# Kernel tuning notes

Hardware: AMD Instinct MI355X
Metric: run time of the kernel (lower is better)

## Reference

```python
import jax, jax.numpy as jnp
import numpy as np

N_HEAD = 8

def setup_inputs() -> dict:
    key = jax.random.key(0)
    ks = jax.random.split(key, 5)
    B, T, C = 2, 4096, 512
    x = jax.random.normal(ks[0], (B, T, C), dtype=jnp.float32)
    w_attn = jax.random.normal(ks[1], (3 * C, C), dtype=jnp.float32) * (1.0 / np.sqrt(C))
    b_attn = jax.random.normal(ks[2], (3 * C,), dtype=jnp.float32) * 0.02
    w_proj = jax.random.normal(ks[3], (C, C), dtype=jnp.float32) * (1.0 / np.sqrt(C))
    b_proj = jax.random.normal(ks[4], (C,), dtype=jnp.float32) * 0.02
    return {"x": x, "w_attn": w_attn, "b_attn": b_attn, "w_proj": w_proj, "b_proj": b_proj}

def reference(x, w_attn, b_attn, w_proj, b_proj):
    B, T, C = x.shape
    H = N_HEAD
    D = C // H  # head dim
    qkv = x @ w_attn.T + b_attn  # [B,T,3C]
    q, k, v = jnp.split(qkv, 3, axis=-1)
    # b t (h d) -> b h t d
    def to_heads(t):
        return t.reshape(B, T, H, D).transpose(0, 2, 1, 3)
    q, k, v = to_heads(q), to_heads(k), to_heads(v)
    scale = 1.0 / np.sqrt(D).astype(np.float32)
    att = jnp.einsum('bhqd,bhkd->bhqk', q, k) * scale  # [B,H,T,T]
    causal = jnp.tril(jnp.ones((T, T), dtype=bool))
    att = jnp.where(causal[None, None], att, jnp.float32(-jnp.inf))
    att = jax.nn.softmax(att, axis=-1)
    y = jnp.einsum('bhqk,bhkd->bhqd', att, v)  # [B,H,T,D]
    y = y.transpose(0, 2, 1, 3).reshape(B, T, C)
    return y @ w_proj.T + b_proj
```

## Files before the change

kernel.cpp:

```cpp
#include <hip/hip_runtime.h>

typedef __attribute__((ext_vector_type(8))) __bf16 bf16x8;
typedef __attribute__((ext_vector_type(4))) __bf16 bf16x4;
typedef __attribute__((ext_vector_type(4))) float f32x4;
typedef __attribute__((ext_vector_type(16))) float f32x16;
typedef __attribute__((ext_vector_type(4))) unsigned uint32x4;

#define AS1 __attribute__((address_space(1)))
#define AS3 __attribute__((address_space(3)))

#if __has_builtin(__builtin_amdgcn_exp2f)
#define EXP2(x) __builtin_amdgcn_exp2f(x)
#else
#define EXP2(x) exp2f(x)
#endif

#define QSCALE 0.18033688011112042f

#define N_X 4194304
#define N_WA 786432
#define N_WP 262144
__global__ __launch_bounds__(256) void convert_all_k(const float* __restrict__ x,
                                                     const float* __restrict__ wa,
                                                     const float* __restrict__ wp,
                                                     __bf16* __restrict__ xb,
                                                     __bf16* __restrict__ wab,
                                                     __bf16* __restrict__ wpb) {
  int i = (blockIdx.x * 256 + threadIdx.x) * 4;
  const float* src;
  __bf16* dst;
  int off;
  if (i < N_X)              { src = x;  dst = xb;  off = i; }
  else if (i < N_X + N_WA)  { src = wa; dst = wab; off = i - N_X; }
  else if (i < N_X + N_WA + N_WP) { src = wp; dst = wpb; off = i - N_X - N_WA; }
  else return;
  float4 v = *reinterpret_cast<const float4*>(src + off);
  bf16x4 o;
  o[0] = (__bf16)v.x; o[1] = (__bf16)v.y; o[2] = (__bf16)v.z; o[3] = (__bf16)v.w;
  *reinterpret_cast<bf16x4*>(dst + off) = o;
}

template <int EPI>
__global__ __launch_bounds__(256) void gemm_bt(const __bf16* __restrict__ A,
                                               const __bf16* __restrict__ Bm,
                                               const float* __restrict__ bias,
                                               void* __restrict__ outp,
                                               __bf16* __restrict__ vtout,
                                               int M, int N, int K) {
  __shared__ __bf16 a_lds[128 * 64];
  __shared__ __bf16 b_lds[128 * 64];
  const int tid = threadIdx.x;
  const int lane = tid & 63;
  const int w = tid >> 6;
  const int wm = w >> 1, wn = w & 1;
  const int ll = lane & 15, lh = lane >> 4;
  const int m0 = blockIdx.y * 128;
  const int n0 = blockIdx.x * 128;
  f32x4 acc[4][4] = {};

  for (int k0 = 0; k0 < K; k0 += 64) {
    __syncthreads();
#pragma unroll
    for (int i = 0; i < 4; ++i) {
      int ch = i * 256 + w * 64 + lane;
      int r = ch >> 3, c8 = ch & 7;
      const __bf16* ga = A + (size_t)(m0 + r) * K + k0 + c8 * 8;
      __builtin_amdgcn_global_load_lds((const AS1 void*)ga,
                                       (AS3 void*)(a_lds + (i * 256 + w * 64) * 8), 16, 0, 0);
      const __bf16* gb = Bm + (size_t)(n0 + r) * K + k0 + c8 * 8;
      __builtin_amdgcn_global_load_lds((const AS1 void*)gb,
                                       (AS3 void*)(b_lds + (i * 256 + w * 64) * 8), 16, 0, 0);
    }
    __syncthreads();
#pragma unroll
    for (int kc = 0; kc < 2; ++kc) {
      bf16x8 af[4], bfr[4];
#pragma unroll
      for (int m = 0; m < 4; ++m)
        af[m] = *reinterpret_cast<const bf16x8*>(a_lds + (wm * 64 + m * 16 + ll) * 64 + kc * 32 + lh * 8);
#pragma unroll
      for (int n = 0; n < 4; ++n)
        bfr[n] = *reinterpret_cast<const bf16x8*>(b_lds + (wn * 64 + n * 16 + ll) * 64 + kc * 32 + lh * 8);
#pragma unroll
      for (int m = 0; m < 4; ++m)
#pragma unroll
        for (int n = 0; n < 4; ++n)
          acc[m][n] = __builtin_amdgcn_mfma_f32_16x16x32_bf16(af[m], bfr[n], acc[m][n], 0, 0, 0);
    }
  }
#pragma unroll
  for (int m = 0; m < 4; ++m) {
    int gm = m0 + wm * 64 + m * 16 + lh * 4;
#pragma unroll
    for (int n = 0; n < 4; ++n) {
      int gn = n0 + wn * 64 + n * 16 + ll;
      float bs = bias[gn];
      float v4[4];
#pragma unroll
      for (int r = 0; r < 4; ++r) v4[r] = acc[m][n][r] + bs;
      if (EPI == 1) {
#pragma unroll
        for (int r = 0; r < 4; ++r)
          ((float*)outp)[(size_t)(gm + r) * N + gn] = v4[r];
      } else if (gn < 1024) {
        float sc = (gn < 512) ? (float)QSCALE : 1.0f;
#pragma unroll
        for (int r = 0; r < 4; ++r)
          ((__bf16*)outp)[(size_t)(gm + r) * N + gn] = (__bf16)(v4[r] * sc);
      } else {
        bf16x4 pk;
#pragma unroll
        for (int r = 0; r < 4; ++r) pk[r] = (__bf16)v4[r];
        *reinterpret_cast<bf16x4*>(vtout + ((size_t)((gm >> 12) * 512 + (gn - 1024))) * 4096 + (gm & 4095)) = pk;
      }
    }
  }
}

struct Tbl { unsigned short t[204]; };
constexpr Tbl build_tbl() {
  Tbl T{};
  int sizes[204] = {};
  int n = 0;
  for (int p = 0; p < 2; ++p)
    for (int qx = 0; qx < 32; ++qx) {
      int total = 2 * qx + 2;
      int nch = (total + 11) / 12;
      int cum = 0;
      for (int q = 0; q < qx; ++q) cum += (2 * q + 13) / 12;
      for (int c = 0; c < nch; ++c) {
        int sz = total - 12 * c; if (sz > 12) sz = 12;
        T.t[n] = (unsigned short)(qx | (c << 5) | (p << 8) | ((cum + c) << 9));
        sizes[n] = sz;
        ++n;
      }
    }
  for (int i = 1; i < n; ++i) {
    unsigned short tv = T.t[i]; int sv = sizes[i];
    int j = i - 1;
    while (j >= 0 && sizes[j] < sv) { T.t[j + 1] = T.t[j]; sizes[j + 1] = sizes[j]; --j; }
    T.t[j + 1] = tv; sizes[j + 1] = sv;
  }
  return T;
}
__device__ __constant__ Tbl g_tbl = build_tbl();

__device__ inline unsigned cvtpk(float lo, float hi_) {
  unsigned r;
  asm("v_cvt_pk_bf16_f32 %0, %1, %2" : "=v"(r) : "v"(lo), "v"(hi_));
  return r;
}

__global__ __launch_bounds__(256, 4) void attn_k(const __bf16* __restrict__ qkv,
                                                 const __bf16* __restrict__ vt,
                                                 __bf16* __restrict__ opart,
                                                 float* __restrict__ lpart) {
  __shared__ __bf16 k_lds[2][64 * 64];
  __shared__ __bf16 v_lds[2][64 * 64];
  const int tid = threadIdx.x, lane = tid & 63, w = tid >> 6;
  const int hi = lane >> 5, q31 = lane & 31;
  const int swz = q31 & 7;

  const int bid = (int)blockIdx.x;
  const int e = g_tbl.t[bid >> 3];
  const int qx = e & 31, c = (e >> 5) & 7, p = (e >> 8) & 1, j = e >> 9;
  const int bh = (bid & 7) * 2 + p;
  const int pslot = bh * 102 + j;
  const int b = bh >> 3, h = bh & 7;
  const int q0 = qx * 128;
  const int qw0 = q0 + w * 32;
  const int t0 = 12 * c;
  const int t1 = min(12 * c + 12, 2 * qx + 2);

  const __bf16* qp = qkv + (size_t)b * 4096 * 1536 + h * 64;
  const __bf16* kp = qp + 512;
  const __bf16* vtp = vt + (size_t)(b * 512 + h * 64) * 4096;

  bf16x8 qf[4];
  {
    const __bf16* qr = qp + (size_t)(qw0 + q31) * 1536 + hi * 8;
#pragma unroll
    for (int d = 0; d < 4; ++d) qf[d] = *reinterpret_cast<const bf16x8*>(qr + d * 16);
  }

  f32x16 o0 = {}, o1 = {};
  float l_run = 0.f;

  auto stage = [&](int tt, int ss) {
    const int kv0s = tt * 64;
#pragma unroll
    for (int i = 0; i < 2; ++i) {
      int ch = i * 256 + tid;
      int r = ch >> 3, cc = ch & 7;
      int cs = cc ^ (r & 7);
      __builtin_amdgcn_global_load_lds(
          (const AS1 void*)(kp + (size_t)(kv0s + r) * 1536 + cs * 8),
          (AS3 void*)(&k_lds[ss][(i * 256 + w * 64) * 8]), 16, 0, 0);
      __builtin_amdgcn_global_load_lds(
          (const AS1 void*)(vtp + (size_t)r * 4096 + kv0s + cs * 8),
          (AS3 void*)(&v_lds[ss][(i * 256 + w * 64) * 8]), 16, 0, 0);
    }
  };

  stage(t0, 0);
  __builtin_amdgcn_sched_barrier(0);

  int slot = 0;
  for (int t = t0; t < t1; ++t) {
    asm volatile("s_waitcnt vmcnt(0)" ::: "memory");
    __builtin_amdgcn_sched_barrier(0);
    __builtin_amdgcn_s_barrier();
    __builtin_amdgcn_sched_barrier(0);
    if (t + 1 < t1) {
      stage(t + 1, slot ^ 1);
      __builtin_amdgcn_sched_barrier(0);
    }
    const int kv0 = t * 64;
    if (kv0 <= qw0 + 31) {
      f32x16 s0 = {}, s1 = {};
      __builtin_amdgcn_s_setprio(1);
#pragma unroll
      for (int d = 0; d < 4; ++d) {
        int c0 = ((d * 2 + hi) ^ swz) * 8;
        s0 = __builtin_amdgcn_mfma_f32_32x32x16_bf16(
            *reinterpret_cast<const bf16x8*>(&k_lds[slot][q31 * 64 + c0]), qf[d], s0, 0, 0, 0);
        s1 = __builtin_amdgcn_mfma_f32_32x32x16_bf16(
            *reinterpret_cast<const bf16x8*>(&k_lds[slot][(32 + q31) * 64 + c0]), qf[d], s1, 0, 0, 0);
      }
      __builtin_amdgcn_s_setprio(0);
      if (kv0 + 63 > qw0) {
        const int q = qw0 + q31;
#pragma unroll
        for (int r = 0; r < 16; ++r) {
          int crow = (r & 3) + 8 * (r >> 2) + 4 * hi;
          if (kv0 + crow > q) s0[r] = -1e30f;
          if (kv0 + 32 + crow > q) s1[r] = -1e30f;
        }
      }
#pragma unroll
      for (int r = 0; r < 16; ++r) s0[r] = EXP2(s0[r]);
#pragma unroll
      for (int r = 0; r < 16; ++r) s1[r] = EXP2(s1[r]);
      float a8[8];
#pragma unroll
      for (int r = 0; r < 8; ++r)
        a8[r] = (s0[r] + s0[r + 8]) + (s1[r] + s1[r + 8]);
#pragma unroll
      for (int st = 4; st >= 1; st >>= 1)
#pragma unroll
        for (int r = 0; r < 4; ++r)
          if (r < st) a8[r] += a8[r + st];
      l_run += a8[0] + __shfl_xor(a8[0], 32);
      uint32x4 pa[4];
#pragma unroll
      for (int half = 0; half < 2; ++half) {
        const int bse = half * 8;
        {
          unsigned x1 = cvtpk(s0[bse + 0], s0[bse + 1]);
          unsigned y1 = cvtpk(s0[bse + 4], s0[bse + 5]);
          asm("v_permlane32_swap_b32 %0, %1" : "+v"(x1), "+v"(y1));
          pa[half][0] = x1; pa[half][2] = y1;
          unsigned x2 = cvtpk(s0[bse + 2], s0[bse + 3]);
          unsigned y2 = cvtpk(s0[bse + 6], s0[bse + 7]);
          asm("v_permlane32_swap_b32 %0, %1" : "+v"(x2), "+v"(y2));
          pa[half][1] = x2; pa[half][3] = y2;
        }
        {
          unsigned x1 = cvtpk(s1[bse + 0], s1[bse + 1]);
          unsigned y1 = cvtpk(s1[bse + 4], s1[bse + 5]);
          asm("v_permlane32_swap_b32 %0, %1" : "+v"(x1), "+v"(y1));
          pa[2 + half][0] = x1; pa[2 + half][2] = y1;
          unsigned x2 = cvtpk(s1[bse + 2], s1[bse + 3]);
          unsigned y2 = cvtpk(s1[bse + 6], s1[bse + 7]);
          asm("v_permlane32_swap_b32 %0, %1" : "+v"(x2), "+v"(y2));
          pa[2 + half][1] = x2; pa[2 + half][3] = y2;
        }
      }
      __builtin_amdgcn_s_setprio(1);
#pragma unroll
      for (int ks = 0; ks < 4; ++ks) {
        int c0 = ((ks * 2 + hi) ^ swz) * 8;
        bf16x8 pfrag = __builtin_bit_cast(bf16x8, pa[ks]);
        o0 = __builtin_amdgcn_mfma_f32_32x32x16_bf16(
            *reinterpret_cast<const bf16x8*>(&v_lds[slot][q31 * 64 + c0]), pfrag, o0, 0, 0, 0);
        o1 = __builtin_amdgcn_mfma_f32_32x32x16_bf16(
            *reinterpret_cast<const bf16x8*>(&v_lds[slot][(32 + q31) * 64 + c0]), pfrag, o1, 0, 0, 0);
      }
      __builtin_amdgcn_s_setprio(0);
    }
    __builtin_amdgcn_sched_barrier(0);
    slot ^= 1;
  }

  const float inv = 1.f / l_run;
  const int rloc = w * 32 + q31;
  __bf16* ob = opart + ((size_t)pslot * 128 + rloc) * 64;
#pragma unroll
  for (int g = 0; g < 4; ++g) {
    bf16x4 v0, v1;
#pragma unroll
    for (int jj = 0; jj < 4; ++jj) {
      v0[jj] = (__bf16)(o0[g * 4 + jj] * inv);
      v1[jj] = (__bf16)(o1[g * 4 + jj] * inv);
    }
    *reinterpret_cast<bf16x4*>(ob + 8 * g + 4 * hi) = v0;
    *reinterpret_cast<bf16x4*>(ob + 32 + 8 * g + 4 * hi) = v1;
  }
  if (hi == 0) lpart[pslot * 128 + rloc] = l_run;
}

__global__ __launch_bounds__(256) void combine_k(const __bf16* __restrict__ opart,
                                                 const float* __restrict__ lpart,
                                                 __bf16* __restrict__ y) {
  const int bid = (int)blockIdx.x;
  const int bh = bid >> 5, qx = bid & 31;
  const int b = bh >> 3, h = bh & 7;
  const int n = (2 * qx + 13) / 12;
  int cum = 0;
  for (int q = 0; q < qx; ++q) cum += (2 * q + 13) / 12;
  const int g0 = bh * 102 + cum;
  const int tid = threadIdx.x;
  const int r = tid >> 1, dh = (tid & 1) * 32;

  float W = 0.f;
  float acc[32] = {};
  for (int i = 0; i < n; ++i) {
    float wi = lpart[(g0 + i) * 128 + r];
    W += wi;
    const __bf16* op = opart + ((size_t)(g0 + i) * 128 + r) * 64 + dh;
#pragma unroll
    for (int jj = 0; jj < 4; ++jj) {
      bf16x8 v = *reinterpret_cast<const bf16x8*>(op + jj * 8);
#pragma unroll
      for (int e = 0; e < 8; ++e) acc[jj * 8 + e] += wi * (float)v[e];
    }
  }
  const float inv = 1.f / W;
  __bf16* yr = y + ((size_t)b * 4096 + qx * 128 + r) * 512 + h * 64 + dh;
#pragma unroll
  for (int jj = 0; jj < 4; ++jj) {
    bf16x8 ov;
#pragma unroll
    for (int e = 0; e < 8; ++e) ov[e] = (__bf16)(acc[jj * 8 + e] * inv);
    *reinterpret_cast<bf16x8*>(yr + jj * 8) = ov;
  }
}

extern "C" void kernel_launch(void* const* d_in, const int* in_sizes, int n_in,
                              void* d_out, int out_size, void* d_ws, size_t ws_size,
                              hipStream_t stream) {
  const float* x      = (const float*)d_in[0];
  const float* w_attn = (const float*)d_in[1];
  const float* b_attn = (const float*)d_in[2];
  const float* w_proj = (const float*)d_in[3];
  const float* b_proj = (const float*)d_in[4];
  float* out = (float*)d_out;

  const int Bv = 2, T = 4096, C = 512;
  const int M = Bv * T;

  const size_t NPART = (size_t)1632 * 128 * 64;
  __bf16* opart  = (__bf16*)d_ws;
  __bf16* x_bf   = opart;
  __bf16* wa_bf  = opart + NPART;
  __bf16* wp_bf  = wa_bf + (size_t)786432;
  __bf16* qkv_bf = wp_bf + (size_t)262144;
  __bf16* y_bf   = qkv_bf + (size_t)12582912;
  __bf16* vt_bf  = y_bf + (size_t)4194304;
  float*  lpart  = (float*)(vt_bf + (size_t)4194304);

  const int ntot = N_X + N_WA + N_WP;
  convert_all_k<<<(ntot / 4 + 255) / 256, 256, 0, stream>>>(x, w_attn, w_proj, x_bf, wa_bf, wp_bf);

  gemm_bt<0><<<dim3(3 * C / 128, M / 128), 256, 0, stream>>>(x_bf, wa_bf, b_attn, qkv_bf, vt_bf, M, 3 * C, C);
  attn_k<<<dim3(1632), 256, 0, stream>>>(qkv_bf, vt_bf, opart, lpart);
  combine_k<<<dim3(512), 256, 0, stream>>>(opart, lpart, y_bf);
  gemm_bt<1><<<dim3(C / 128, M / 128), 256, 0, stream>>>(y_bf, wp_bf, b_proj, out, nullptr, M, C, C);
}
```

Before: 115.1 us.

## Load V from global into registers, pair KV tiles, coalesce QKV epilogue, skip combine

The attention kernel stops staging V through LDS. Each wave reads its V^T fragments straight from global memory into registers. K is now staged two 64-row tiles per barrier phase, and occupancy is lowered to 3 blocks. Query blocks whose whole key range fits in a single chunk write normalized output directly to y, so combine_k skips them. Separately, the QKV GEMM epilogue for Q/K now goes through LDS to emit coalesced 16-byte stores. The trade-off is extra register pressure and uncached global V reads in place of LDS sharing across waves.

```diff
diff --git a/kernel.cpp b/kernel.cpp
--- a/kernel.cpp
+++ b/kernel.cpp
@@ -88,29 +88,50 @@
           acc[m][n] = __builtin_amdgcn_mfma_f32_16x16x32_bf16(af[m], bfr[n], acc[m][n], 0, 0, 0);
     }
   }
-#pragma unroll
-  for (int m = 0; m < 4; ++m) {
-    int gm = m0 + wm * 64 + m * 16 + lh * 4;
-#pragma unroll
-    for (int n = 0; n < 4; ++n) {
-      int gn = n0 + wn * 64 + n * 16 + ll;
-      float bs = bias[gn];
-      float v4[4];
-#pragma unroll
-      for (int r = 0; r < 4; ++r) v4[r] = acc[m][n][r] + bs;
-      if (EPI == 1) {
+  if (EPI == 1) {
+#pragma unroll
+    for (int m = 0; m < 4; ++m) {
+      int gm = m0 + wm * 64 + m * 16 + lh * 4;
+#pragma unroll
+      for (int n = 0; n < 4; ++n) {
+        int gn = n0 + wn * 64 + n * 16 + ll;
+        float bs = bias[gn];
 #pragma unroll
         for (int r = 0; r < 4; ++r)
-          ((float*)outp)[(size_t)(gm + r) * N + gn] = v4[r];
-      } else if (gn < 1024) {
-        float sc = (gn < 512) ? (float)QSCALE : 1.0f;
+          ((float*)outp)[(size_t)(gm + r) * N + gn] = acc[m][n][r] + bs;
+      }
+    }
+  } else if (n0 < 1024) {
+    __syncthreads();
+    __bf16* tb = (w < 2 ? a_lds : b_lds) + (w & 1) * 4096;
+    const float sc = (n0 < 512) ? (float)QSCALE : 1.0f;
+#pragma unroll
+    for (int m = 0; m < 4; ++m)
+#pragma unroll
+      for (int n = 0; n < 4; ++n) {
+        float bs = bias[n0 + wn * 64 + n * 16 + ll];
 #pragma unroll
         for (int r = 0; r < 4; ++r)
-          ((__bf16*)outp)[(size_t)(gm + r) * N + gn] = (__bf16)(v4[r] * sc);
-      } else {
+          tb[(m * 16 + lh * 4 + r) * 64 + n * 16 + ll] = (__bf16)((acc[m][n][r] + bs) * sc);
+      }
+    const int rsub = lane >> 3, csub = (lane & 7) * 8;
+#pragma unroll
+    for (int i = 0; i < 8; ++i) {
+      bf16x8 vv = *reinterpret_cast<const bf16x8*>(tb + (i * 8 + rsub) * 64 + csub);
+      *reinterpret_cast<bf16x8*>((__bf16*)outp +
+          (size_t)(m0 + wm * 64 + i * 8 + rsub) * N + n0 + wn * 64 + csub) = vv;
+    }
+  } else {
+#pragma unroll
+    for (int m = 0; m < 4; ++m) {
+      int gm = m0 + wm * 64 + m * 16 + lh * 4;
+#pragma unroll
+      for (int n = 0; n < 4; ++n) {
+        int gn = n0 + wn * 64 + n * 16 + ll;
+        float bs = bias[gn];
         bf16x4 pk;
 #pragma unroll
-        for (int r = 0; r < 4; ++r) pk[r] = (__bf16)v4[r];
+        for (int r = 0; r < 4; ++r) pk[r] = (__bf16)(acc[m][n][r] + bs);
         *reinterpret_cast<bf16x4*>(vtout + ((size_t)((gm >> 12) * 512 + (gn - 1024))) * 4096 + (gm & 4095)) = pk;
       }
     }
@@ -151,12 +172,12 @@
   return r;
 }
 
-__global__ __launch_bounds__(256, 4) void attn_k(const __bf16* __restrict__ qkv,
+__global__ __launch_bounds__(256, 3) void attn_k(const __bf16* __restrict__ qkv,
                                                  const __bf16* __restrict__ vt,
                                                  __bf16* __restrict__ opart,
-                                                 float* __restrict__ lpart) {
-  __shared__ __bf16 k_lds[2][64 * 64];
-  __shared__ __bf16 v_lds[2][64 * 64];
+                                                 float* __restrict__ lpart,
+                                                 __bf16* __restrict__ y) {
+  __shared__ __bf16 k_lds[2][2][64 * 64];
   const int tid = threadIdx.x, lane = tid & 63, w = tid >> 6;
   const int hi = lane >> 5, q31 = lane & 31;
   const int swz = q31 & 7;
@@ -171,10 +192,13 @@
   const int qw0 = q0 + w * 32;
   const int t0 = 12 * c;
   const int t1 = min(12 * c + 12, 2 * qx + 2);
+  const int p0 = t0 >> 1, p1 = t1 >> 1;
 
   const __bf16* qp = qkv + (size_t)b * 4096 * 1536 + h * 64;
   const __bf16* kp = qp + 512;
   const __bf16* vtp = vt + (size_t)(b * 512 + h * 64) * 4096;
+  const __bf16* v0p = vtp + (size_t)q31 * 4096 + hi * 8;
+  const __bf16* v1p = vtp + (size_t)(32 + q31) * 4096 + hi * 8;
 
   bf16x8 qf[4];
   {
@@ -186,7 +210,7 @@
   f32x16 o0 = {}, o1 = {};
   float l_run = 0.f;
 
-  auto stage = [&](int tt, int ss) {
+  auto stageK = [&](int tt, int ss, int half) {
     const int kv0s = tt * 64;
 #pragma unroll
     for (int i = 0; i < 2; ++i) {
@@ -195,118 +219,148 @@
       int cs = cc ^ (r & 7);
       __builtin_amdgcn_global_load_lds(
           (const AS1 void*)(kp + (size_t)(kv0s + r) * 1536 + cs * 8),
-          (AS3 void*)(&k_lds[ss][(i * 256 + w * 64) * 8]), 16, 0, 0);
-      __builtin_amdgcn_global_load_lds(
-          (const AS1 void*)(vtp + (size_t)r * 4096 + kv0s + cs * 8),
-          (AS3 void*)(&v_lds[ss][(i * 256 + w * 64) * 8]), 16, 0, 0);
+          (AS3 void*)(&k_lds[ss][half][(i * 256 + w * 64) * 8]), 16, 0, 0);
     }
   };
 
-  stage(t0, 0);
+  auto tile = [&](const __bf16* kb, int kv0, uint32x4* vv) {
+    f32x16 s0 = {}, s1 = {};
+    __builtin_amdgcn_s_setprio(1);
+#pragma unroll
+    for (int d = 0; d < 4; ++d) {
+      int c0 = ((d * 2 + hi) ^ swz) * 8;
+      s0 = __builtin_amdgcn_mfma_f32_32x32x16_bf16(
+          *reinterpret_cast<const bf16x8*>(kb + q31 * 64 + c0), qf[d], s0, 0, 0, 0);
+      s1 = __builtin_amdgcn_mfma_f32_32x32x16_bf16(
+          *reinterpret_cast<const bf16x8*>(kb + (32 + q31) * 64 + c0), qf[d], s1, 0, 0, 0);
+    }
+    __builtin_amdgcn_s_setprio(0);
+    if (kv0 + 63 > qw0) {
+      const int q = qw0 + q31;
+#pragma unroll
+      for (int r = 0; r < 16; ++r) {
+        int crow = (r & 3) + 8 * (r >> 2) + 4 * hi;
+        if (kv0 + crow > q) s0[r] = -1e30f;
+        if (kv0 + 32 + crow > q) s1[r] = -1e30f;
+      }
+    }
+#pragma unroll
+    for (int r = 0; r < 16; ++r) s0[r] = EXP2(s0[r]);
+#pragma unroll
+    for (int r = 0; r < 16; ++r) s1[r] = EXP2(s1[r]);
+    float a8[8];
+#pragma unroll
+    for (int r = 0; r < 8; ++r)
+      a8[r] = (s0[r] + s0[r + 8]) + (s1[r] + s1[r + 8]);
+#pragma unroll
+    for (int st = 4; st >= 1; st >>= 1)
+#pragma unroll
+      for (int r = 0; r < 4; ++r)
+        if (r < st) a8[r] += a8[r + st];
+    l_run += a8[0] + __shfl_xor(a8[0], 32);
+    uint32x4 pa[4];
+#pragma unroll
+    for (int half = 0; half < 2; ++half) {
+      const int bse = half * 8;
+      {
+        unsigned x1 = cvtpk(s0[bse + 0], s0[bse + 1]);
+        unsigned y1 = cvtpk(s0[bse + 4], s0[bse + 5]);
+        asm("v_permlane32_swap_b32 %0, %1" : "+v"(x1), "+v"(y1));
+        pa[half][0] = x1; pa[half][2] = y1;
+        unsigned x2 = cvtpk(s0[bse + 2], s0[bse + 3]);
+        unsigned y2 = cvtpk(s0[bse + 6], s0[bse + 7]);
+        asm("v_permlane32_swap_b32 %0, %1" : "+v"(x2), "+v"(y2));
+        pa[half][1] = x2; pa[half][3] = y2;
+      }
+      {
+        unsigned x1 = cvtpk(s1[bse + 0], s1[bse + 1]);
+        unsigned y1 = cvtpk(s1[bse + 4], s1[bse + 5]);
+        asm("v_permlane32_swap_b32 %0, %1" : "+v"(x1), "+v"(y1));
+        pa[2 + half][0] = x1; pa[2 + half][2] = y1;
+        unsigned x2 = cvtpk(s1[bse + 2], s1[bse + 3]);
+        unsigned y2 = cvtpk(s1[bse + 6], s1[bse + 7]);
+        asm("v_permlane32_swap_b32 %0, %1" : "+v"(x2), "+v"(y2));
+        pa[2 + half][1] = x2; pa[2 + half][3] = y2;
+      }
+    }
+    __builtin_amdgcn_s_setprio(1);
+#pragma unroll
+    for (int ks = 0; ks < 4; ++ks) {
+      bf16x8 pfrag = __builtin_bit_cast(bf16x8, pa[ks]);
+      o0 = __builtin_amdgcn_mfma_f32_32x32x16_bf16(
+          __builtin_bit_cast(bf16x8, vv[ks]), pfrag, o0, 0, 0, 0);
+      o1 = __builtin_amdgcn_mfma_f32_32x32x16_bf16(
+          __builtin_bit_cast(bf16x8, vv[4 + ks]), pfrag, o1, 0, 0, 0);
+    }
+    __builtin_amdgcn_s_setprio(0);
+  };
+
+  stageK(2 * p0, 0, 0);
+  stageK(2 * p0 + 1, 0, 1);
   __builtin_amdgcn_sched_barrier(0);
 
   int slot = 0;
-  for (int t = t0; t < t1; ++t) {
+  for (int ph = p0; ph < p1; ++ph) {
     asm volatile("s_waitcnt vmcnt(0)" ::: "memory");
     __builtin_amdgcn_sched_barrier(0);
     __builtin_amdgcn_s_barrier();
     __builtin_amdgcn_sched_barrier(0);
-    if (t + 1 < t1) {
-      stage(t + 1, slot ^ 1);
+    const int tA = 2 * ph;
+    const int kvA = tA * 64, kvB = kvA + 64;
+    uint32x4 vv[8];
+#pragma unroll
+    for (int ks = 0; ks < 4; ++ks) {
+      vv[ks] = *reinterpret_cast<const uint32x4*>(v0p + kvA + ks * 16);
+      vv[4 + ks] = *reinterpret_cast<const uint32x4*>(v1p + kvA + ks * 16);
+    }
+    __builtin_amdgcn_sched_barrier(0);
+    if (ph + 1 < p1) {
+      stageK(tA + 2, slot ^ 1, 0);
+      stageK(tA + 3, slot ^ 1, 1);
       __builtin_amdgcn_sched_barrier(0);
     }
-    const int kv0 = t * 64;
-    if (kv0 <= qw0 + 31) {
-      f32x16 s0 = {}, s1 = {};
-      __builtin_amdgcn_s_setprio(1);
-#pragma unroll
-      for (int d = 0; d < 4; ++d) {
-        int c0 = ((d * 2 + hi) ^ swz) * 8;
-        s0 = __builtin_amdgcn_mfma_f32_32x32x16_bf16(
-            *reinterpret_cast<const bf16x8*>(&k_lds[slot][q31 * 64 + c0]), qf[d], s0, 0, 0, 0);
-        s1 = __builtin_amdgcn_mfma_f32_32x32x16_bf16(
-            *reinterpret_cast<const bf16x8*>(&k_lds[slot][(32 + q31) * 64 + c0]), qf[d], s1, 0, 0, 0);
-      }
-      __builtin_amdgcn_s_setprio(0);
-      if (kv0 + 63 > qw0) {
-        const int q = qw0 + q31;
-#pragma unroll
-        for (int r = 0; r < 16; ++r) {
-          int crow = (r & 3) + 8 * (r >> 2) + 4 * hi;
-          if (kv0 + crow > q) s0[r] = -1e30f;
-          if (kv0 + 32 + crow > q) s1[r] = -1e30f;
-        }
-      }
-#pragma unroll
-      for (int r = 0; r < 16; ++r) s0[r] = EXP2(s0[r]);
-#pragma unroll
-      for (int r = 0; r < 16; ++r) s1[r] = EXP2(s1[r]);
-      float a8[8];
-#pragma unroll
-      for (int r = 0; r < 8; ++r)
-        a8[r] = (s0[r] + s0[r + 8]) + (s1[r] + s1[r + 8]);
-#pragma unroll
-      for (int st = 4; st >= 1; st >>= 1)
-#pragma unroll
-        for (int r = 0; r < 4; ++r)
-          if (r < st) a8[r] += a8[r + st];
-      l_run += a8[0] + __shfl_xor(a8[0], 32);
-      uint32x4 pa[4];
-#pragma unroll
-      for (int half = 0; half < 2; ++half) {
-        const int bse = half * 8;
-        {
-          unsigned x1 = cvtpk(s0[bse + 0], s0[bse + 1]);
-          unsigned y1 = cvtpk(s0[bse + 4], s0[bse + 5]);
-          asm("v_permlane32_swap_b32 %0, %1" : "+v"(x1), "+v"(y1));
-          pa[half][0] = x1; pa[half][2] = y1;
-          unsigned x2 = cvtpk(s0[bse + 2], s0[bse + 3]);
-          unsigned y2 = cvtpk(s0[bse + 6], s0[bse + 7]);
-          asm("v_permlane32_swap_b32 %0, %1" : "+v"(x2), "+v"(y2));
-          pa[half][1] = x2; pa[half][3] = y2;
-        }
-        {
-          unsigned x1 = cvtpk(s1[bse + 0], s1[bse + 1]);
-          unsigned y1 = cvtpk(s1[bse + 4], s1[bse + 5]);
-          asm("v_permlane32_swap_b32 %0, %1" : "+v"(x1), "+v"(y1));
-          pa[2 + half][0] = x1; pa[2 + half][2] = y1;
-          unsigned x2 = cvtpk(s1[bse + 2], s1[bse + 3]);
-          unsigned y2 = cvtpk(s1[bse + 6], s1[bse + 7]);
-          asm("v_permlane32_swap_b32 %0, %1" : "+v"(x2), "+v"(y2));
-          pa[2 + half][1] = x2; pa[2 + half][3] = y2;
-        }
-      }
-      __builtin_amdgcn_s_setprio(1);
+    if (kvA <= qw0 + 31) tile(&k_lds[slot][0][0], kvA, vv);
+    if (kvB <= qw0 + 31) {
 #pragma unroll
       for (int ks = 0; ks < 4; ++ks) {
-        int c0 = ((ks * 2 + hi) ^ swz) * 8;
-        bf16x8 pfrag = __builtin_bit_cast(bf16x8, pa[ks]);
-        o0 = __builtin_amdgcn_mfma_f32_32x32x16_bf16(
-            *reinterpret_cast<const bf16x8*>(&v_lds[slot][q31 * 64 + c0]), pfrag, o0, 0, 0, 0);
-        o1 = __builtin_amdgcn_mfma_f32_32x32x16_bf16(
-            *reinterpret_cast<const bf16x8*>(&v_lds[slot][(32 + q31) * 64 + c0]), pfrag, o1, 0, 0, 0);
-      }
-      __builtin_amdgcn_s_setprio(0);
-    }
-    __builtin_amdgcn_sched_barrier(0);
+        vv[ks] = *reinterpret_cast<const uint32x4*>(v0p + kvB + ks * 16);
+        vv[4 + ks] = *reinterpret_cast<const uint32x4*>(v1p + kvB + ks * 16);
+      }
+      tile(&k_lds[slot][1][0], kvB, vv);
+    }
     slot ^= 1;
   }
 
   const float inv = 1.f / l_run;
   const int rloc = w * 32 + q31;
-  __bf16* ob = opart + ((size_t)pslot * 128 + rloc) * 64;
-#pragma unroll
-  for (int g = 0; g < 4; ++g) {
-    bf16x4 v0, v1;
-#pragma unroll
-    for (int jj = 0; jj < 4; ++jj) {
-      v0[jj] = (__bf16)(o0[g * 4 + jj] * inv);
-      v1[jj] = (__bf16)(o1[g * 4 + jj] * inv);
-    }
-    *reinterpret_cast<bf16x4*>(ob + 8 * g + 4 * hi) = v0;
-    *reinterpret_cast<bf16x4*>(ob + 32 + 8 * g + 4 * hi) = v1;
-  }
-  if (hi == 0) lpart[pslot * 128 + rloc] = l_run;
+  if (t0 == 0 && t1 == 2 * qx + 2) {
+    __bf16* yr = y + ((size_t)b * 4096 + qw0 + q31) * 512 + h * 64;
+#pragma unroll
+    for (int g = 0; g < 4; ++g) {
+      bf16x4 v0, v1;
+#pragma unroll
+      for (int jj = 0; jj < 4; ++jj) {
+        v0[jj] = (__bf16)(o0[g * 4 + jj] * inv);
+        v1[jj] = (__bf16)(o1[g * 4 + jj] * inv);
+      }
+      *reinterpret_cast<bf16x4*>(yr + 8 * g + 4 * hi) = v0;
+      *reinterpret_cast<bf16x4*>(yr + 32 + 8 * g + 4 * hi) = v1;
+    }
+  } else {
+    __bf16* ob = opart + ((size_t)pslot * 128 + rloc) * 64;
+#pragma unroll
+    for (int g = 0; g < 4; ++g) {
+      bf16x4 v0, v1;
+#pragma unroll
+      for (int jj = 0; jj < 4; ++jj) {
+        v0[jj] = (__bf16)(o0[g * 4 + jj] * inv);
+        v1[jj] = (__bf16)(o1[g * 4 + jj] * inv);
+      }
+      *reinterpret_cast<bf16x4*>(ob + 8 * g + 4 * hi) = v0;
+      *reinterpret_cast<bf16x4*>(ob + 32 + 8 * g + 4 * hi) = v1;
+    }
+    if (hi == 0) lpart[pslot * 128 + rloc] = l_run;
+  }
 }
 
 __global__ __launch_bounds__(256) void combine_k(const __bf16* __restrict__ opart,
@@ -314,6 +368,7 @@
                                                  __bf16* __restrict__ y) {
   const int bid = (int)blockIdx.x;
   const int bh = bid >> 5, qx = bid & 31;
+  if (qx < 6) return;
   const int b = bh >> 3, h = bh & 7;
   const int n = (2 * qx + 13) / 12;
   int cum = 0;
@@ -373,7 +428,7 @@
   convert_all_k<<<(ntot / 4 + 255) / 256, 256, 0, stream>>>(x, w_attn, w_proj, x_bf, wa_bf, wp_bf);
 
   gemm_bt<0><<<dim3(3 * C / 128, M / 128), 256, 0, stream>>>(x_bf, wa_bf, b_attn, qkv_bf, vt_bf, M, 3 * C, C);
-  attn_k<<<dim3(1632), 256, 0, stream>>>(qkv_bf, vt_bf, opart, lpart);
+  attn_k<<<dim3(1632), 256, 0, stream>>>(qkv_bf, vt_bf, opart, lpart, y_bf);
   combine_k<<<dim3(512), 256, 0, stream>>>(opart, lpart, y_bf);
   gemm_bt<1><<<dim3(C / 128, M / 128), 256, 0, stream>>>(y_bf, wp_bf, b_proj, out, nullptr, M, C, C);
 }
```

Measured after the change: 146.2 us. 27.0% more time.
